# Optimization experiments

Hardware: AMD Instinct MI355X
Metric: run time of the kernel (lower is better)

The kernel has to match this reference:

```python
import jax, jax.numpy as jnp
import numpy as np

CHEB_K = 3

def _cheb(A, K):
    # Chebyshev polynomials T0=I, T1=A, Tk=2*A@T(k-1)-T(k-2); A: [...,N,N]
    N = A.shape[-1]
    I = jnp.broadcast_to(jnp.eye(N, dtype=A.dtype), A.shape)
    polys = [I, A]
    for _ in range(2, K):
        polys.append(2.0 * jnp.matmul(A, polys[-1]) - polys[-2])
    return jnp.stack(polys[:K], axis=-3)  # [...,K,N,N]

def _agcn(x, graphs, W, b):
    # x: [B,N,C]; graphs: [K,N,N] (static) or [B,K,N,N] (dynamic)
    if graphs.ndim == 3:
        xg = jnp.einsum('knm,bmc->bnkc', graphs, x)
    else:
        xg = jnp.einsum('bknm,bmc->bnkc', graphs, x)
    B, N = x.shape[0], x.shape[1]
    xg = xg.reshape(B, N, -1)  # concat over cheb order, matching torch cat order
    return jnp.einsum('bni,io->bno', xg, W) + b

def _gru_step(x_t, state, graphs, gW, gb, uW, ub, hidden):
    inp = jnp.concatenate([x_t, state], axis=-1)
    zr = jax.nn.sigmoid(_agcn(inp, graphs, gW, gb))
    z, r = zr[..., :hidden], zr[..., hidden:]
    cand = jnp.concatenate([x_t, z * state], axis=-1)
    hc = jnp.tanh(_agcn(cand, graphs, uW, ub))
    return r * state + (1.0 - r) * hc

def setup_inputs():
    key = jax.random.key(0)
    ks = jax.random.split(key, 16)
    B, T, N, D = 32, 12, 512, 1
    H, E, K = 64, 10, CHEB_K
    ycov, out_d = 1, 1
    def w(k, shape, s=0.1):
        return jax.random.normal(k, shape, dtype=jnp.float32) * s
    enc_in = D + H
    dec_in = out_d + ycov + H
    return dict(
        x=jax.random.normal(ks[0], (B, T, N, D), dtype=jnp.float32),
        y_cov=jax.random.uniform(ks[1], (B, T, N, ycov), dtype=jnp.float32),
        node_embeddings=w(ks[2], (N, E), 1.0),
        enc_gate_W=w(ks[3], (K * enc_in, 2 * H)),
        enc_gate_b=jnp.zeros((2 * H,), jnp.float32),
        enc_upd_W=w(ks[4], (K * enc_in, H)),
        enc_upd_b=jnp.zeros((H,), jnp.float32),
        dec_gate_W=w(ks[5], (K * dec_in, 2 * H)),
        dec_gate_b=jnp.zeros((2 * H,), jnp.float32),
        dec_upd_W=w(ks[6], (K * dec_in, H)),
        dec_upd_b=jnp.zeros((H,), jnp.float32),
        proj_W=w(ks[7], (H, out_d)),
        proj_b=jnp.zeros((out_d,), jnp.float32),
        hyper_W=w(ks[8], (H, E)),
        hyper_b=jnp.zeros((E,), jnp.float32),
    )

def reference(x, y_cov, node_embeddings, enc_gate_W, enc_gate_b, enc_upd_W, enc_upd_b,
              dec_gate_W, dec_gate_b, dec_upd_W, dec_upd_b, proj_W, proj_b,
              hyper_W, hyper_b):
    B, T, N, D = x.shape
    H = enc_upd_W.shape[-1]
    K = CHEB_K
    # static adaptive support from node embeddings
    A = jax.nn.softmax(jax.nn.relu(node_embeddings @ node_embeddings.T), axis=-1)
    graphs_s = _cheb(A, K)  # [K,N,N]
    h0 = jnp.zeros((B, N, H), x.dtype)
    def enc_step(h, x_t):
        h = _gru_step(x_t, h, graphs_s, enc_gate_W, enc_gate_b, enc_upd_W, enc_upd_b, H)
        return h, None
    h_t, _ = jax.lax.scan(enc_step, h0, jnp.swapaxes(x, 0, 1))
    # dynamic (batch-wise) support via hypernet on the final encoder state
    E_dyn = node_embeddings[None] + (h_t @ hyper_W + hyper_b)  # [B,N,E]
    A_d = jax.nn.softmax(jax.nn.relu(jnp.einsum('bne,bme->bnm', E_dyn, E_dyn)), axis=-1)
    graphs_d = _cheb(A_d, K)  # [B,K,N,N]
    go0 = jnp.zeros((B, N, proj_W.shape[-1]), x.dtype)
    def dec_step(carry, yc_t):
        h, go = carry
        x_t = jnp.concatenate([go, yc_t], axis=-1)
        h = _gru_step(x_t, h, graphs_d, dec_gate_W, dec_gate_b, dec_upd_W, dec_upd_b, H)
        go = h @ proj_W + proj_b
        return (h, go), go
    _, outs = jax.lax.scan(dec_step, (h_t, go0), jnp.swapaxes(y_cov, 0, 1))
    return jnp.swapaxes(outs, 0, 1)  # [B, horizon, N, out_dim]
```

## Files before the change

### kernel.cpp

```cpp
#include <hip/hip_runtime.h>

#define NB 32
#define TT 12
#define NN 512
#define HH 64
#define EE 10
#define XS 80
#define KD 240
#define RS (NB*NN)
#define TTNN (TT*NN)
#define GP 164

typedef _Float16 f16;
typedef __attribute__((ext_vector_type(4))) _Float16 f16x4;
typedef __attribute__((ext_vector_type(8))) _Float16 f16x8;
typedef __attribute__((ext_vector_type(4))) float f32x4;

#define MFMA32(a,bb,c) __builtin_amdgcn_mfma_f32_16x16x32_f16(a,bb,c,0,0,0)
#define MFMA16(a,bb,c) __builtin_amdgcn_mfma_f32_16x16x16f16(a,bb,c,0,0,0)

__device__ __forceinline__ void barrier_lgkm() {
  asm volatile("s_waitcnt lgkmcnt(0)" ::: "memory");
  __builtin_amdgcn_s_barrier();
  __builtin_amdgcn_sched_barrier(0);
}

union SMem {
  struct {
    f16 PsH[2][2][64][32];
    f16 XtH[2][80][40];
  } s1;
  struct {
    f16 gH[64][GP];
  } s2;
};

__global__ void fold_w_t(const float* __restrict__ src, f16* __restrict__ WtH,
                         int C, int O){
  int idx = blockIdx.x*256 + threadIdx.x;
  if (idx >= O*KD) return;
  int o = idx / KD;
  int k = idx % KD;
  int s = k / XS, c = k % XS;
  float v = 0.f;
  if (c < C) {
    if (s == 0)      v = src[c*O+o] - src[(2*C+c)*O+o];
    else if (s == 1) v = src[(C+c)*O+o];
    else             v = 2.f*src[(2*C+c)*O+o];
  }
  WtH[idx] = (f16)v;
}

__global__ __launch_bounds__(512) void softmax_graph(
    const float* __restrict__ Emb, long long ebs,
    f16* __restrict__ AH, long long abs_)
{
  __shared__ float Es[NN*EE];
  int b  = blockIdx.x >> 6;
  int rt = blockIdx.x & 63;
  const float* Eb = Emb + (long long)b*ebs;
  int tid = threadIdx.x;
  for (int i = tid; i < NN*EE; i += 512) Es[i] = Eb[i];
  __syncthreads();
  int wave = tid >> 6, lane = tid & 63;
  int r = rt*8 + wave;
  float q[EE];
  #pragma unroll
  for (int e = 0; e < EE; ++e) q[e] = Es[r*EE + e];
  float sv[8];
  float mx = 0.f;
  #pragma unroll
  for (int j = 0; j < 8; ++j) {
    int m = 64*j + lane;
    float s = 0.f;
    #pragma unroll
    for (int e = 0; e < EE; ++e) s += q[e]*Es[m*EE + e];
    s = fmaxf(s, 0.f);
    sv[j] = s;
    mx = fmaxf(mx, s);
  }
  #pragma unroll
  for (int off = 32; off >= 1; off >>= 1) mx = fmaxf(mx, __shfl_xor(mx, off, 64));
  float sm = 0.f;
  #pragma unroll
  for (int j = 0; j < 8; ++j) { sv[j] = expf(sv[j] - mx); sm += sv[j]; }
  #pragma unroll
  for (int off = 32; off >= 1; off >>= 1) sm += __shfl_xor(sm, off, 64);
  float inv = 1.f / sm;
  #pragma unroll
  for (int j = 0; j < 8; ++j) {
    int m = 64*j + lane;
    AH[(long long)b*abs_ + (long long)r*NN + m] = (f16)(sv[j] * inv);
  }
}

__global__ __launch_bounds__(256) void sq_mm(
    const f16* __restrict__ AH, long long astr,
    f16* __restrict__ BH, long long bstr)
{
  __shared__ f16 RsH[64][36], CsH[64][34];
  int b = blockIdx.z;
  int rows0 = blockIdx.y*64, cols0 = blockIdx.x*64;
  const f16* Ah = AH + (long long)b*astr;
  int tid = threadIdx.x, l = tid & 63, w = tid >> 6, lr = l & 15, lg = l >> 4;
  int ar = w*16 + lr;
  int st_row = tid >> 2, st_seg = tid & 3;
  int sx_m = tid >> 3, sx_sub = tid & 7;
  f32x4 acc[4] = {};
  for (int kt = 0; kt < 16; ++kt) {
    int k0 = kt*32;
    barrier_lgkm();
    {
      f16x8 vh = *(const f16x8*)&Ah[(long long)(rows0+st_row)*NN + k0 + 8*st_seg];
      *(f16x8*)&RsH[st_row][8*st_seg] = vh;
    }
    #pragma unroll
    for (int j = 0; j < 2; ++j) {
      int c4 = sx_sub + 8*j;
      f16x4 vh = *(const f16x4*)&Ah[(long long)(k0+sx_m)*NN + cols0 + 4*c4];
      #pragma unroll
      for (int q = 0; q < 4; ++q)
        CsH[4*c4+q][sx_m] = vh[q];
    }
    barrier_lgkm();
    f16x8 a_h = *(const f16x8*)&RsH[ar][8*lg];
    #pragma unroll
    for (int cf = 0; cf < 4; ++cf) {
      int c = cf*16 + lr;
      f16x8 b_h = *(const f16x8*)&CsH[c][8*lg];
      acc[cf] = MFMA32(a_h, b_h, acc[cf]);
    }
  }
  #pragma unroll
  for (int cf = 0; cf < 4; ++cf) {
    #pragma unroll
    for (int reg = 0; reg < 4; ++reg) {
      int r = rows0 + w*16 + lg*4 + reg;
      int c = cols0 + cf*16 + lr;
      BH[(long long)b*bstr + (long long)r*NN + c] = (f16)acc[cf][reg];
    }
  }
}

__global__ void fill_col(f16* __restrict__ XRH, f16* __restrict__ XCH, int col,
                         const float* __restrict__ src, long long sstr){
  int row = blockIdx.x*256 + threadIdx.x;
  if (row >= RS) return;
  float v = src[(long long)(row>>9)*sstr + (row & 511)];
  f16 hi = (f16)v;
  XRH[(long long)row*XS + col] = hi;
  XCH[(long long)col*RS + row] = hi;
}

template<int GATE, int DEC>
__global__ __launch_bounds__(512, 2) void fused_half(
    const f16* __restrict__ AH, const f16* __restrict__ A2H, long long astr,
    const f16* __restrict__ XiRH, const f16* __restrict__ XiCH,
    f16* __restrict__ XoRH, f16* __restrict__ XoCH,
    const f16* __restrict__ WH,
    const float* __restrict__ bias,
    float* __restrict__ hbuf, float* __restrict__ rb,
    const float* __restrict__ pWv, const float* __restrict__ pbv,
    float* __restrict__ outp, int t,
    const float* __restrict__ s0src, const float* __restrict__ s1src,
    int ns, int ns_next, int writeX)
{
  __shared__ SMem sm;
  __shared__ float gpart[64];
  const int b = blockIdx.x;
  const int rows0 = blockIdx.y * 64;
  const long long bNN = (long long)b*NN;
  const int tid = threadIdx.x;
  const int w = tid >> 6, l = tid & 63;
  const int lr = l & 15, lg = l >> 4;
  const int grp = w >> 2;
  const int w4 = w & 3;
  const int ar = w4*16 + lr;
  const int asw = (ar >> 2) & 3;

  const int stw = (tid < 256) ? 0 : 1;
  const int at = tid & 255;
  const int st_row = at >> 2, st_seg = at & 3;
  const int a_sw = (st_row >> 2) & 3;
  const f16* PgH = (stw ? A2H : AH) + (long long)b*astr + (long long)rows0*NN;

  const int xc = tid >> 2;
  const int xo = tid & 3;
  const int xok = (xc < 80);
  const f16* XC1 = XiCH + (long long)(xok ? xc : 0)*RS + bNN;

  f16x8 rH0{}, x10{}, rH1{}, x11{};

  auto LOAD = [&](int kt, f16x8& rH, f16x8& x1){
    int k0 = kt*32;
    rH = *(const f16x8*)&PgH[(long long)st_row*NN + k0 + 8*st_seg];
    if (xok) x1 = *(const f16x8*)&XC1[k0 + 8*xo];
  };
  auto STORE = [&](int buf, f16x8& rH, f16x8& x1){
    *(f16x8*)&sm.s1.PsH[buf][stw][st_row][8*(st_seg ^ a_sw)] = rH;
    if (xok) *(f16x8*)&sm.s1.XtH[buf][xc][8*xo] = x1;
  };
  f32x4 acc[5] = {};
  auto COMP = [&](int buf){
    f16x8 ah = *(const f16x8*)&sm.s1.PsH[buf][grp][ar][8*(lg ^ asw)];
    __builtin_amdgcn_s_setprio(1);
    #pragma unroll
    for (int cf = 0; cf < 5; ++cf) {
      int c = cf*16 + lr;
      f16x8 bh = *(const f16x8*)&sm.s1.XtH[buf][c][8*lg];
      acc[cf] = MFMA32(ah, bh, acc[cf]);
    }
    __builtin_amdgcn_s_setprio(0);
  };

  LOAD(0, rH0,x10);
  LOAD(1, rH1,x11);
  STORE(0, rH0,x10);
  barrier_lgkm();
  #pragma unroll
  for (int kt2 = 0; kt2 < 8; ++kt2) {
    int kt = kt2*2;
    if (kt+2 < 16) LOAD(kt+2, rH0,x10);
    COMP(0);
    STORE(1, rH1,x11);
    barrier_lgkm();
    if (kt+3 < 16) LOAD(kt+3, rH1,x11);
    COMP(1);
    if (kt+2 < 16) STORE(0, rH0,x10);
    barrier_lgkm();
  }

  {
    int go_ = grp*80;
    #pragma unroll
    for (int cf = 0; cf < 5; ++cf) {
      int col = go_ + cf*16 + lr;
      #pragma unroll
      for (int reg = 0; reg < 4; ++reg) {
        int row = w4*16 + lg*4 + reg;
        sm.s2.gH[row][col] = (f16)acc[cf][reg];
      }
    }
  }
  barrier_lgkm();

  constexpr int CFW = GATE ? 4 : 2;
  f32x4 accD[CFW] = {};
  const long long grow0 = bNN + rows0 + w4*16;
  const f16* xrH = XiRH + (grow0 + lr)*XS;
  #pragma unroll
  for (int c = 0; c < 15; ++c) {
    f16x4 a_h;
    if (c < 5) {
      a_h = *(const f16x4*)&xrH[c*16 + 4*lg];
    } else {
      a_h = *(const f16x4*)&sm.s2.gH[w4*16 + lr][(c-5)*16 + 4*lg];
    }
    #pragma unroll
    for (int cf = 0; cf < CFW; ++cf) {
      int o = grp*(CFW*16) + cf*16 + lr;
      f16x4 b_h = *(const f16x4*)&WH[(long long)o*KD + c*16 + 4*lg];
      accD[cf] = MFMA16(a_h, b_h, accD[cf]);
    }
  }

  if constexpr (GATE) {
    #pragma unroll
    for (int cf = 0; cf < CFW; ++cf) {
      int o = grp*64 + cf*16 + lr;
      float bi = bias[o];
      #pragma unroll
      for (int reg = 0; reg < 4; ++reg) {
        long long grow = grow0 + lg*4 + reg;
        float v = 1.f/(1.f + expf(-(accD[cf][reg] + bi)));
        if (grp == 0) {
          float zh = v * hbuf[grow*HH + o];
          f16 hi = (f16)zh;
          XoRH[grow*XS + ns + o] = hi;
          XoCH[(long long)(ns+o)*RS + grow] = hi;
        } else {
          rb[grow*HH + (o - HH)] = v;
        }
      }
    }
    if (grp == 0 && lr < ns) {
      #pragma unroll
      for (int reg = 0; reg < 4; ++reg) {
        long long grow = grow0 + lg*4 + reg;
        f16 vh = XiRH[grow*XS + lr];
        XoRH[grow*XS + lr] = vh;
        XoCH[(long long)lr*RS + grow] = vh;
      }
    }
  } else {
    float gop[4] = {0.f,0.f,0.f,0.f};
    #pragma unroll
    for (int cf = 0; cf < CFW; ++cf) {
      int o = grp*32 + cf*16 + lr;
      float bi = bias[o];
      float pwv = 0.f;
      if constexpr (DEC) pwv = pWv[o];
      #pragma unroll
      for (int reg = 0; reg < 4; ++reg) {
        long long grow = grow0 + lg*4 + reg;
        float hc = tanhf(accD[cf][reg] + bi);
        float rv = rb[grow*HH + o];
        float hv = hbuf[grow*HH + o];
        float hn = rv*hv + (1.f - rv)*hc;
        hbuf[grow*HH + o] = hn;
        if (writeX) {
          f16 hi = (f16)hn;
          XoRH[grow*XS + ns_next + o] = hi;
          XoCH[(long long)(ns_next+o)*RS + grow] = hi;
        }
        if constexpr (DEC) gop[reg] += hn * pwv;
      }
    }
    if constexpr (DEC) {
      #pragma unroll
      for (int reg = 0; reg < 4; ++reg) {
        #pragma unroll
        for (int off = 8; off >= 1; off >>= 1)
          gop[reg] += __shfl_xor(gop[reg], off, 64);
      }
      if (grp == 1 && lr == 0) {
        #pragma unroll
        for (int reg = 0; reg < 4; ++reg)
          gpart[w4*16 + lg*4 + reg] = gop[reg];
      }
      barrier_lgkm();
      if (grp == 0 && lr == 0) {
        float pb0 = pbv[0];
        #pragma unroll
        for (int reg = 0; reg < 4; ++reg) {
          int n = rows0 + w4*16 + lg*4 + reg;
          long long grow = bNN + n;
          float go = gop[reg] + gpart[w4*16 + lg*4 + reg] + pb0;
          outp[((long long)b*TT + t)*NN + n] = go;
          if (writeX) {
            f16 hi = (f16)go;
            XoRH[grow*XS] = hi;
            XoCH[grow] = hi;
            float yv = s1src[(long long)b*TTNN + n];
            f16 hy = (f16)yv;
            XoRH[grow*XS + 1] = hy;
            XoCH[RS + grow] = hy;
          }
        }
      }
    } else {
      if (writeX && grp == 0 && lr == 0) {
        #pragma unroll
        for (int reg = 0; reg < 4; ++reg) {
          int n = rows0 + w4*16 + lg*4 + reg;
          long long grow = bNN + n;
          float v0 = s0src ? s0src[(long long)b*TTNN + n] : 0.f;
          f16 h0 = (f16)v0;
          XoRH[grow*XS] = h0;
          XoCH[grow] = h0;
          if (ns_next == 2 && s1src) {
            float v1 = s1src[(long long)b*TTNN + n];
            f16 h1 = (f16)v1;
            XoRH[grow*XS + 1] = h1;
            XoCH[RS + grow] = h1;
          }
        }
      }
    }
  }
}

__global__ __launch_bounds__(256) void edyn_k(
    const float* __restrict__ h, const float* __restrict__ ne,
    const float* __restrict__ hW, const float* __restrict__ hb, float* __restrict__ Ed)
{
  int row = blockIdx.x*4 + (threadIdx.x >> 6);
  int lane = threadIdx.x & 63;
  float hv = h[(long long)row*HH + lane];
  float myval = 0.f;
  #pragma unroll
  for (int e = 0; e < EE; ++e) {
    float v = hv * hW[lane*EE + e];
    #pragma unroll
    for (int off = 32; off >= 1; off >>= 1) v += __shfl_xor(v, off, 64);
    if (lane == e) myval = v;
  }
  if (lane < EE) {
    int n = row & 511;
    Ed[(long long)row*EE + lane] = ne[n*EE + lane] + hb[lane] + myval;
  }
}

extern "C" void kernel_launch(void* const* d_in, const int* in_sizes, int n_in,
                              void* d_out, int out_size, void* d_ws, size_t ws_size,
                              hipStream_t stream)
{
  const float* x    = (const float*)d_in[0];
  const float* ycov = (const float*)d_in[1];
  const float* ne   = (const float*)d_in[2];
  const float* egW  = (const float*)d_in[3];
  const float* egb  = (const float*)d_in[4];
  const float* euW  = (const float*)d_in[5];
  const float* eub  = (const float*)d_in[6];
  const float* dgW  = (const float*)d_in[7];
  const float* dgb  = (const float*)d_in[8];
  const float* duW  = (const float*)d_in[9];
  const float* dub  = (const float*)d_in[10];
  const float* pW   = (const float*)d_in[11];
  const float* pb   = (const float*)d_in[12];
  const float* hW   = (const float*)d_in[13];
  const float* hb   = (const float*)d_in[14];
  float* out = (float*)d_out;

  char* p = (char*)d_ws;
  f16* AsH  = (f16*)p; p += (size_t)NN*NN*2;
  f16* As2H = (f16*)p; p += (size_t)NN*NN*2;
  f16* AdH  = (f16*)p; p += (size_t)NB*NN*NN*2;
  f16* Ad2H = (f16*)p; p += (size_t)NB*NN*NN*2;
  f16* XaRH = (f16*)p; p += (size_t)RS*XS*2;
  f16* XaCH = (f16*)p; p += (size_t)RS*XS*2;
  f16* XbRH = (f16*)p; p += (size_t)RS*XS*2;
  f16* XbCH = (f16*)p; p += (size_t)RS*XS*2;
  float* h  = (float*)p; p += (size_t)RS*HH*4;
  float* rb = (float*)p; p += (size_t)RS*HH*4;
  float* Ed = (float*)p; p += (size_t)RS*EE*4;
  f16* WgeH = (f16*)p; p += (size_t)128*KD*2;
  f16* WueH = (f16*)p; p += (size_t)64*KD*2;
  f16* WgdH = (f16*)p; p += (size_t)128*KD*2;
  f16* WudH = (f16*)p; p += (size_t)64*KD*2;

  fold_w_t<<<(128*KD+255)/256, 256, 0, stream>>>(egW, WgeH, 65, 128);
  fold_w_t<<<(64*KD +255)/256, 256, 0, stream>>>(euW, WueH, 65, 64);
  fold_w_t<<<(128*KD+255)/256, 256, 0, stream>>>(dgW, WgdH, 66, 128);
  fold_w_t<<<(64*KD +255)/256, 256, 0, stream>>>(duW, WudH, 66, 64);

  softmax_graph<<<64, 512, 0, stream>>>(ne, 0, AsH, 0);
  sq_mm<<<dim3(8,8,1), 256, 0, stream>>>(AsH, 0, As2H, 0);
  (void)hipMemsetAsync(h, 0, (size_t)RS*HH*4, stream);
  (void)hipMemsetAsync(XaRH, 0, (size_t)RS*XS*2*4, stream);
  fill_col<<<(RS+255)/256, 256, 0, stream>>>(XaRH, XaCH, 0, x, (long long)TTNN);

  dim3 fgrid(NB, 8);
  for (int t = 0; t < TT; ++t) {
    fused_half<1,0><<<fgrid, 512, 0, stream>>>(
        AsH, As2H, 0,
        XaRH, XaCH, XbRH, XbCH,
        WgeH, egb, h, rb, nullptr, nullptr, nullptr, t,
        nullptr, nullptr, 1, 0, 1);
    fused_half<0,0><<<fgrid, 512, 0, stream>>>(
        AsH, As2H, 0,
        XbRH, XbCH, XaRH, XaCH,
        WueH, eub, h, rb, nullptr, nullptr, nullptr, t,
        (t < TT-1 ? x + (size_t)(t+1)*NN : nullptr),
        (t < TT-1 ? nullptr : ycov),
        1, (t < TT-1 ? 1 : 2), 1);
  }

  edyn_k<<<RS/4, 256, 0, stream>>>(h, ne, hW, hb, Ed);
  softmax_graph<<<NB*64, 512, 0, stream>>>(Ed, (long long)NN*EE, AdH, (long long)NN*NN);
  sq_mm<<<dim3(8,8,NB), 256, 0, stream>>>(AdH, (long long)NN*NN, Ad2H, (long long)NN*NN);

  for (int t = 0; t < TT; ++t) {
    fused_half<1,0><<<fgrid, 512, 0, stream>>>(
        AdH, Ad2H, (long long)NN*NN,
        XaRH, XaCH, XbRH, XbCH,
        WgdH, dgb, h, rb, nullptr, nullptr, nullptr, t,
        nullptr, nullptr, 2, 0, 1);
    fused_half<0,1><<<fgrid, 512, 0, stream>>>(
        AdH, Ad2H, (long long)NN*NN,
        XbRH, XbCH, XaRH, XaCH,
        WudH, dub, h, rb, pW, pb, out, t,
        nullptr, (t < TT-1 ? ycov + (size_t)(t+1)*NN : nullptr),
        2, 2, (t < TT-1 ? 1 : 0));
  }
}
```

Before: 1.022 ms.

## Load graph-operator fragments straight into registers instead of staging via LDS

Each warp now preloads its full 16-step strip of the Chebyshev graph-operator matrix into registers (16 f16x8 per lane) up front, rather than double-buffering it through shared memory. Only the X tile is still staged through LDS, with a reworked single-step pipeline. This cuts shared-memory traffic, LDS footprint, and the A store and load in every K step. The cost is much higher register pressure, which could lower occupancy, and all A loads are issued at once instead of being overlapped with compute.

```diff
diff --git a/kernel.cpp b/kernel.cpp
--- a/kernel.cpp
+++ b/kernel.cpp
@@ -26,13 +26,8 @@
 }
 
 union SMem {
-  struct {
-    f16 PsH[2][2][64][32];
-    f16 XtH[2][80][40];
-  } s1;
-  struct {
-    f16 gH[64][GP];
-  } s2;
+  f16 XtH[2][80][40];
+  f16 gH[64][GP];
 };
 
 __global__ void fold_w_t(const float* __restrict__ src, f16* __restrict__ WtH,
@@ -176,57 +171,55 @@
   const int grp = w >> 2;
   const int w4 = w & 3;
   const int ar = w4*16 + lr;
-  const int asw = (ar >> 2) & 3;
-
-  const int stw = (tid < 256) ? 0 : 1;
-  const int at = tid & 255;
-  const int st_row = at >> 2, st_seg = at & 3;
-  const int a_sw = (st_row >> 2) & 3;
-  const f16* PgH = (stw ? A2H : AH) + (long long)b*astr + (long long)rows0*NN;
+
+  f16x8 aF[16];
+  {
+    const f16* Ag = (grp ? A2H : AH) + (long long)b*astr
+                  + (long long)(rows0 + ar)*NN + 8*lg;
+    #pragma unroll
+    for (int kt = 0; kt < 16; ++kt)
+      aF[kt] = *(const f16x8*)&Ag[kt*32];
+  }
 
   const int xc = tid >> 2;
   const int xo = tid & 3;
   const int xok = (xc < 80);
   const f16* XC1 = XiCH + (long long)(xok ? xc : 0)*RS + bNN;
 
-  f16x8 rH0{}, x10{}, rH1{}, x11{};
-
-  auto LOAD = [&](int kt, f16x8& rH, f16x8& x1){
-    int k0 = kt*32;
-    rH = *(const f16x8*)&PgH[(long long)st_row*NN + k0 + 8*st_seg];
-    if (xok) x1 = *(const f16x8*)&XC1[k0 + 8*xo];
+  f16x8 xr0{}, xr1{};
+
+  auto LOADX = [&](int kt, f16x8& x1){
+    if (xok) x1 = *(const f16x8*)&XC1[kt*32 + 8*xo];
   };
-  auto STORE = [&](int buf, f16x8& rH, f16x8& x1){
-    *(f16x8*)&sm.s1.PsH[buf][stw][st_row][8*(st_seg ^ a_sw)] = rH;
-    if (xok) *(f16x8*)&sm.s1.XtH[buf][xc][8*xo] = x1;
+  auto STOREX = [&](int buf, f16x8& x1){
+    if (xok) *(f16x8*)&sm.XtH[buf][xc][8*xo] = x1;
   };
   f32x4 acc[5] = {};
-  auto COMP = [&](int buf){
-    f16x8 ah = *(const f16x8*)&sm.s1.PsH[buf][grp][ar][8*(lg ^ asw)];
+  auto COMP = [&](int buf, f16x8 ah){
     __builtin_amdgcn_s_setprio(1);
     #pragma unroll
     for (int cf = 0; cf < 5; ++cf) {
       int c = cf*16 + lr;
-      f16x8 bh = *(const f16x8*)&sm.s1.XtH[buf][c][8*lg];
+      f16x8 bh = *(const f16x8*)&sm.XtH[buf][c][8*lg];
       acc[cf] = MFMA32(ah, bh, acc[cf]);
     }
     __builtin_amdgcn_s_setprio(0);
   };
 
-  LOAD(0, rH0,x10);
-  LOAD(1, rH1,x11);
-  STORE(0, rH0,x10);
+  LOADX(0, xr0);
+  LOADX(1, xr1);
+  STOREX(0, xr0);
   barrier_lgkm();
   #pragma unroll
-  for (int kt2 = 0; kt2 < 8; ++kt2) {
-    int kt = kt2*2;
-    if (kt+2 < 16) LOAD(kt+2, rH0,x10);
-    COMP(0);
-    STORE(1, rH1,x11);
-    barrier_lgkm();
-    if (kt+3 < 16) LOAD(kt+3, rH1,x11);
-    COMP(1);
-    if (kt+2 < 16) STORE(0, rH0,x10);
+  for (int kt = 0; kt < 16; ++kt) {
+    const int cur = kt & 1;
+    if (kt+1 < 16) {
+      if (cur == 0) STOREX(1, xr1); else STOREX(0, xr0);
+    }
+    if (kt+2 < 16) {
+      if (cur == 0) LOADX(kt+2, xr0); else LOADX(kt+2, xr1);
+    }
+    COMP(cur, aF[kt]);
     barrier_lgkm();
   }
 
@@ -238,7 +231,7 @@
       #pragma unroll
       for (int reg = 0; reg < 4; ++reg) {
         int row = w4*16 + lg*4 + reg;
-        sm.s2.gH[row][col] = (f16)acc[cf][reg];
+        sm.gH[row][col] = (f16)acc[cf][reg];
       }
     }
   }
@@ -254,7 +247,7 @@
     if (c < 5) {
       a_h = *(const f16x4*)&xrH[c*16 + 4*lg];
     } else {
-      a_h = *(const f16x4*)&sm.s2.gH[w4*16 + lr][(c-5)*16 + 4*lg];
+      a_h = *(const f16x4*)&sm.gH[w4*16 + lr][(c-5)*16 + 4*lg];
     }
     #pragma unroll
     for (int cf = 0; cf < CFW; ++cf) {
```

New measurement: 1.102 ms. +7.8%, slower.
